# Kernel tuning notes

Hardware: AMD Instinct MI355X
Metric: run time of the kernel (lower is better)

Reference implementation:

```python
import jax, jax.numpy as jnp
import numpy as np

D_MODEL = 2048
N_HEAD = 16
N_QUERY = 2
D_HEAD = D_MODEL // (N_HEAD * N_QUERY)  # 64
KV_DIM = D_HEAD * N_HEAD                # 1024
ROPE_BASE = 10000.0


def rope(x):
    """Interleaved RoPE. theta denominator uses the RoPE module's d_model/2
    (full D_MODEL), and only the first D/2 frequencies are used for inputs of
    last dim D < D_MODEL (as in the torch code's theta[..., :d_model_2])."""
    d2_full = D_MODEL // 2
    theta = ROPE_BASE ** (-jnp.arange(d2_full, dtype=jnp.float32) / d2_full)
    S, D = x.shape[-2], x.shape[-1]
    d2 = D // 2
    ang = jnp.arange(S, dtype=jnp.float32)[:, None] * theta[:d2]  # (S, d2)
    cos, sin = jnp.cos(ang), jnp.sin(ang)
    e, o = x[..., 0::2], x[..., 1::2]
    # interleave rotated even/odd back into original layout
    return jnp.stack([e * cos - o * sin, o * cos + e * sin], axis=-1).reshape(x.shape)


def setup_inputs() -> dict:
    key = jax.random.key(0)
    ks = jax.random.split(key, 5)
    x = jax.random.normal(ks[0], (2, 2048, D_MODEL), dtype=jnp.float32)
    # weights stored as (in, out) so forward is x @ W
    Wq = jax.random.normal(ks[1], (D_MODEL, D_MODEL), dtype=jnp.float32) * 0.02
    Wk = jax.random.normal(ks[2], (D_MODEL, KV_DIM), dtype=jnp.float32) * 0.02
    Wv = jax.random.normal(ks[3], (D_MODEL, KV_DIM), dtype=jnp.float32) * 0.02
    Wo = jax.random.normal(ks[4], (D_MODEL, D_MODEL), dtype=jnp.float32) * 0.02
    return {"x": x, "Wq": Wq, "Wk": Wk, "Wv": Wv, "Wo": Wo}


def reference(x, Wq, Wk, Wv, Wo):
    b, s, _ = x.shape
    q = rope(x @ Wq)          # (b, s, D_MODEL)
    k = rope(x @ Wk)          # (b, s, KV_DIM)
    v = x @ Wv                # (b, s, KV_DIM)
    # query heads: flat head index h = g*N_QUERY + q_idx (g indexes KV head group)
    q = q.reshape(b, s, N_HEAD, N_QUERY, D_HEAD).transpose(0, 2, 3, 1, 4)  # (b,h,q,s,d)
    k = k.reshape(b, s, N_HEAD, D_HEAD)  # (b,t,h,d)
    v = v.reshape(b, s, N_HEAD, D_HEAD)
    scale = 1.0 / jnp.sqrt(jnp.asarray(D_HEAD, dtype=jnp.float32))
    scores = jnp.einsum('bhqsd,bthd->bhqst', q, k) * scale  # (b,h,q,s,t)
    probs = jax.nn.softmax(scores, axis=-1)
    out = jnp.einsum('bhqst,bthd->bhqsd', probs, v)         # (b,h,q,s,d)
    out = out.transpose(0, 3, 1, 2, 4).reshape(b, s, D_MODEL)  # (b,s,h*q*d)
    return out @ Wo
```

## Files before the change

### kernel.cpp

```cpp
#include <hip/hip_runtime.h>
#include <hip/hip_bf16.h>
#include <math.h>

#define D_MODEL 2048
#define KV_DIM  1024
#define N_HEAD  16
#define N_QUERY 2
#define D_HEAD  64
#define BATCH   2
#define SEQ     2048
#define MROWS   (BATCH * SEQ)

typedef __attribute__((ext_vector_type(8))) short short8x;
typedef __attribute__((ext_vector_type(4))) float f32x4;

__device__ __forceinline__ short f2bf_rn(float f) {
    unsigned u = __float_as_uint(f);
    unsigned r = (u + 0x7fffu + ((u >> 16) & 1u)) >> 16;
    return (short)r;
}
__device__ __forceinline__ float bf2f(short s) {
    return __uint_as_float(((unsigned)(unsigned short)s) << 16);
}

__device__ __forceinline__ void gload_lds16(const short* g, short* l) {
    __builtin_amdgcn_global_load_lds(
        (const __attribute__((address_space(1))) void*)g,
        (__attribute__((address_space(3))) void*)l,
        16, 0, 0);
}

__global__ __launch_bounds__(256)
void split_kernel(const float* __restrict__ in, short* __restrict__ h,
                  short* __restrict__ l, int n) {
    const int i = (blockIdx.x * 256 + threadIdx.x) * 4;
    if (i >= n) return;
    float4 v = *(const float4*)&in[i];
    short4 hv, lv;
    hv.x = f2bf_rn(v.x); lv.x = f2bf_rn(v.x - bf2f(hv.x));
    hv.y = f2bf_rn(v.y); lv.y = f2bf_rn(v.y - bf2f(hv.y));
    hv.z = f2bf_rn(v.z); lv.z = f2bf_rn(v.z - bf2f(hv.z));
    hv.w = f2bf_rn(v.w); lv.w = f2bf_rn(v.w - bf2f(hv.w));
    *(short4*)&h[i] = hv;
    *(short4*)&l[i] = lv;
}

__global__ __launch_bounds__(256)
void split_tr_kernel(const float* __restrict__ in, short* __restrict__ h,
                     short* __restrict__ l, int K, int N) {
    __shared__ float t[32][33];
    const int k0 = blockIdx.y * 32;
    const int n0 = blockIdx.x * 32;
    const int c  = threadIdx.x & 31;
    const int r0 = threadIdx.x >> 5;
#pragma unroll
    for (int i = 0; i < 4; ++i) {
        const int r = r0 + i * 8;
        t[r][c] = in[(size_t)(k0 + r) * N + n0 + c];
    }
    __syncthreads();
#pragma unroll
    for (int i = 0; i < 4; ++i) {
        const int r = r0 + i * 8;
        const float f = t[c][r];
        const short hb = f2bf_rn(f);
        const size_t off = (size_t)(n0 + r) * K + k0 + c;
        h[off] = hb;
        l[off] = f2bf_rn(f - bf2f(hb));
    }
}

template <int MODE>
__global__ __launch_bounds__(256)
void mgemm_bf_kernel(const short* __restrict__ Ah_g, const short* __restrict__ Al_g,
                     const short* __restrict__ Bth_g, const short* __restrict__ Btl_g,
                     float* __restrict__ C, short* __restrict__ Ch, short* __restrict__ Cl,
                     int M, int N, int K) {
    __shared__ __align__(16) short Ah[128 * 64];
    __shared__ __align__(16) short Al[128 * 64];
    __shared__ __align__(16) short Bh[128 * 64];
    __shared__ __align__(16) short Bl[128 * 64];

    const int tid  = threadIdx.x;
    const int lane = tid & 63;
    const int wid  = tid >> 6;
    const int wm   = (wid >> 1) * 64;
    const int wn   = (wid & 1) * 64;
    const int row0 = blockIdx.y * 128;
    const int col0 = blockIdx.x * 128;
    const int arow = lane & 15;
    const int kg   = lane >> 4;

    f32x4 acc[4][4];
#pragma unroll
    for (int m = 0; m < 4; ++m)
#pragma unroll
        for (int n = 0; n < 4; ++n) acc[m][n] = (f32x4)0.f;

    for (int kt = 0; kt < K; kt += 64) {
#pragma unroll
        for (int i = 0; i < 4; ++i) {
            const int c   = i * 256 + tid;
            const int r   = c >> 3;
            const int kc  = c & 7;
            const int kcs = kc ^ (r & 7);
            const int db  = (i * 256 + (tid & 192)) * 8;
            const size_t sa = (size_t)(row0 + r) * K + kt + kcs * 8;
            const size_t sb = (size_t)(col0 + r) * K + kt + kcs * 8;
            gload_lds16(&Ah_g[sa],  &Ah[db]);
            gload_lds16(&Al_g[sa],  &Al[db]);
            gload_lds16(&Bth_g[sb], &Bh[db]);
            gload_lds16(&Btl_g[sb], &Bl[db]);
        }
        __syncthreads();

#pragma unroll
        for (int kk = 0; kk < 2; ++kk) {
            const int kcb = kk * 4 + kg;
            short8x ah[4], al[4];
#pragma unroll
            for (int m = 0; m < 4; ++m) {
                const int r   = wm + m * 16 + arow;
                const int idx = r * 64 + ((kcb ^ (r & 7)) << 3);
                ah[m] = *(const short8x*)&Ah[idx];
                al[m] = *(const short8x*)&Al[idx];
            }
#pragma unroll
            for (int n = 0; n < 4; ++n) {
                const int rb   = wn + n * 16 + arow;
                const int idxb = rb * 64 + ((kcb ^ (rb & 7)) << 3);
                short8x bh = *(const short8x*)&Bh[idxb];
                short8x bl = *(const short8x*)&Bl[idxb];
#pragma unroll
                for (int m = 0; m < 4; ++m) {
                    acc[m][n] = __builtin_amdgcn_mfma_f32_16x16x32_bf16(ah[m], bl, acc[m][n], 0, 0, 0);
                    acc[m][n] = __builtin_amdgcn_mfma_f32_16x16x32_bf16(al[m], bh, acc[m][n], 0, 0, 0);
                    acc[m][n] = __builtin_amdgcn_mfma_f32_16x16x32_bf16(ah[m], bh, acc[m][n], 0, 0, 0);
                }
            }
        }
        __syncthreads();
    }

#pragma unroll
    for (int m = 0; m < 4; ++m)
#pragma unroll
        for (int n = 0; n < 4; ++n) {
            const int row = row0 + wm + m * 16 + (lane >> 4) * 4;
            const int col = col0 + wn + n * 16 + (lane & 15);
            if (MODE == 2) {
                const float v0 = acc[m][n][0], v1 = acc[m][n][1];
                const float v2 = acc[m][n][2], v3 = acc[m][n][3];
                const short h0 = f2bf_rn(v0), h1 = f2bf_rn(v1);
                const short h2 = f2bf_rn(v2), h3 = f2bf_rn(v3);
                const size_t off = (size_t)col * M + row;
                *(short4*)&Ch[off] = make_short4(h0, h1, h2, h3);
                *(short4*)&Cl[off] = make_short4(
                    f2bf_rn(v0 - bf2f(h0)), f2bf_rn(v1 - bf2f(h1)),
                    f2bf_rn(v2 - bf2f(h2)), f2bf_rn(v3 - bf2f(h3)));
            } else {
#pragma unroll
                for (int j = 0; j < 4; ++j) {
                    const size_t off = (size_t)(row + j) * N + col;
                    if (MODE == 1) {
                        const float val = acc[m][n][j];
                        const short hb = f2bf_rn(val);
                        Ch[off] = hb;
                        Cl[off] = f2bf_rn(val - bf2f(hb));
                    } else {
                        C[off] = acc[m][n][j];
                    }
                }
            }
        }
}

template <int NC, int D2>
__global__ __launch_bounds__(256)
void rope_split_kernel(short* __restrict__ h, short* __restrict__ l) {
    const int idx = blockIdx.x * 256 + threadIdx.x;
    if (idx >= MROWS * D2) return;
    const int row = idx / D2;
    const int j   = idx - row * D2;
    const int pos = row & (SEQ - 1);
    const float theta = __expf(-(float)j * (9.210340371976184f / 1024.0f));
    float s, c;
    sincosf((float)pos * theta, &s, &c);
    const size_t base = (size_t)row * NC + 2 * j;
    short2 hh = *(short2*)&h[base];
    short2 ll = *(short2*)&l[base];
    const float e = bf2f(hh.x) + bf2f(ll.x);
    const float o = bf2f(hh.y) + bf2f(ll.y);
    const float re = e * c - o * s;
    const float ro = o * c + e * s;
    const short rh0 = f2bf_rn(re), rh1 = f2bf_rn(ro);
    *(short2*)&h[base] = make_short2(rh0, rh1);
    *(short2*)&l[base] = make_short2(f2bf_rn(re - bf2f(rh0)), f2bf_rn(ro - bf2f(rh1)));
}

__global__ __launch_bounds__(256)
void attn_mfma_kernel(const short* __restrict__ qh_g, const short* __restrict__ ql_g,
                      const short* __restrict__ kh_g, const short* __restrict__ kl_g,
                      const short* __restrict__ vth_g, const short* __restrict__ vtl_g,
                      short* __restrict__ aoh, short* __restrict__ aol) {
    __shared__ __align__(16) short Qh[64 * 128], Ql[64 * 128];
    __shared__ __align__(16) short Kh[64 * 64], Kl[64 * 64];
    __shared__ __align__(16) short Vth[64 * 64], Vtl[64 * 64];
    __shared__ __align__(16) short Ph[4][16 * 64], Pl[4][16 * 64];

    const int tid  = threadIdx.x;
    const int lane = tid & 63;
    const int wid  = tid >> 6;
    const int wq   = wid * 16;
    const int arow = lane & 15;
    const int kg   = lane >> 4;

    const int y  = blockIdx.y;
    const int b  = y >> 4;
    const int h  = y & 15;
    const int qrow0 = b * SEQ + blockIdx.x * 64;
    const int hcol0 = h * (N_QUERY * D_HEAD);
    const int kvcol = h * D_HEAD;

#pragma unroll
    for (int i = 0; i < 4; ++i) {
        const int c    = i * 256 + tid;
        const int r    = c >> 4;
        const int kc2  = c & 15;
        const int kcs2 = kc2 ^ (r & 7);
        const int db   = (i * 256 + (tid & 192)) * 8;
        const size_t src = (size_t)(qrow0 + r) * D_MODEL + hcol0 + kcs2 * 8;
        gload_lds16(&qh_g[src], &Qh[db]);
        gload_lds16(&ql_g[src], &Ql[db]);
    }

    f32x4 oacc[2][4];
    float mrow[2][4], lrow[2][4];
#pragma unroll
    for (int nq = 0; nq < 2; ++nq)
#pragma unroll
        for (int t = 0; t < 4; ++t) {
            oacc[nq][t] = (f32x4)0.f;
            mrow[nq][t] = -1e30f;
            lrow[nq][t] = 0.f;
        }
    const float scale = 0.125f;
    const size_t kvrow0 = (size_t)b * SEQ;

    for (int tt = 0; tt < SEQ / 64; ++tt) {
        __syncthreads();
#pragma unroll
        for (int i = 0; i < 2; ++i) {
            const int c   = i * 256 + tid;
            const int r   = c >> 3;
            const int kc  = c & 7;
            const int kcs = kc ^ (r & 7);
            const int db  = (i * 256 + (tid & 192)) * 8;
            const size_t sk = (kvrow0 + tt * 64 + r) * KV_DIM + kvcol + kcs * 8;
            const size_t sv = (size_t)(kvcol + r) * MROWS + kvrow0 + tt * 64 + kcs * 8;
            gload_lds16(&kh_g[sk],  &Kh[db]);
            gload_lds16(&kl_g[sk],  &Kl[db]);
            gload_lds16(&vth_g[sv], &Vth[db]);
            gload_lds16(&vtl_g[sv], &Vtl[db]);
        }
        __syncthreads();

#pragma unroll
        for (int nq = 0; nq < 2; ++nq) {
            f32x4 sacc[4];
#pragma unroll
            for (int t = 0; t < 4; ++t) sacc[t] = (f32x4)0.f;
#pragma unroll
            for (int kk = 0; kk < 2; ++kk) {
                const int kcb = kk * 4 + kg;
                const int rq  = wq + arow;
                const int ia  = rq * 128 + nq * 64 + ((kcb ^ (rq & 7)) << 3);
                const short8x qh = *(const short8x*)&Qh[ia];
                const short8x ql = *(const short8x*)&Ql[ia];
#pragma unroll
                for (int t = 0; t < 4; ++t) {
                    const int rk = t * 16 + arow;
                    const int ib = rk * 64 + ((kcb ^ (rk & 7)) << 3);
                    const short8x kh = *(const short8x*)&Kh[ib];
                    const short8x kl = *(const short8x*)&Kl[ib];
                    sacc[t] = __builtin_amdgcn_mfma_f32_16x16x32_bf16(qh, kl, sacc[t], 0, 0, 0);
                    sacc[t] = __builtin_amdgcn_mfma_f32_16x16x32_bf16(ql, kh, sacc[t], 0, 0, 0);
                    sacc[t] = __builtin_amdgcn_mfma_f32_16x16x32_bf16(qh, kh, sacc[t], 0, 0, 0);
                }
            }

            float pv[4][4];
#pragma unroll
            for (int jj = 0; jj < 4; ++jj) {
                float mx = sacc[0][jj] * scale;
#pragma unroll
                for (int t = 1; t < 4; ++t) mx = fmaxf(mx, sacc[t][jj] * scale);
                mx = fmaxf(mx, __shfl_xor(mx, 1));
                mx = fmaxf(mx, __shfl_xor(mx, 2));
                mx = fmaxf(mx, __shfl_xor(mx, 4));
                mx = fmaxf(mx, __shfl_xor(mx, 8));
                const float mnew  = fmaxf(mrow[nq][jj], mx);
                const float alpha = __expf(mrow[nq][jj] - mnew);
                float ls = 0.f;
#pragma unroll
                for (int t = 0; t < 4; ++t) {
                    float p = __expf(sacc[t][jj] * scale - mnew);
                    pv[t][jj] = p;
                    ls += p;
                }
                ls += __shfl_xor(ls, 1);
                ls += __shfl_xor(ls, 2);
                ls += __shfl_xor(ls, 4);
                ls += __shfl_xor(ls, 8);
                lrow[nq][jj] = lrow[nq][jj] * alpha + ls;
                mrow[nq][jj] = mnew;
#pragma unroll
                for (int t = 0; t < 4; ++t) oacc[nq][t][jj] *= alpha;
            }

#pragma unroll
            for (int t = 0; t < 4; ++t)
#pragma unroll
                for (int jj = 0; jj < 4; ++jj) {
                    const int qq  = (lane >> 4) * 4 + jj;
                    const int kv  = t * 16 + (lane & 15);
                    const int idx = qq * 64 + (((kv >> 3) ^ (qq & 7)) << 3) + (kv & 7);
                    const short hb = f2bf_rn(pv[t][jj]);
                    Ph[wid][idx] = hb;
                    Pl[wid][idx] = f2bf_rn(pv[t][jj] - bf2f(hb));
                }
            asm volatile("s_waitcnt lgkmcnt(0)" ::: "memory");

#pragma unroll
            for (int kk = 0; kk < 2; ++kk) {
                const int kcb = kk * 4 + kg;
                const int ip  = arow * 64 + ((kcb ^ (arow & 7)) << 3);
                const short8x ph = *(const short8x*)&Ph[wid][ip];
                const short8x pl = *(const short8x*)&Pl[wid][ip];
#pragma unroll
                for (int t = 0; t < 4; ++t) {
                    const int rv = t * 16 + arow;
                    const int iv = rv * 64 + ((kcb ^ (rv & 7)) << 3);
                    const short8x vh = *(const short8x*)&Vth[iv];
                    const short8x vl = *(const short8x*)&Vtl[iv];
                    oacc[nq][t] = __builtin_amdgcn_mfma_f32_16x16x32_bf16(ph, vl, oacc[nq][t], 0, 0, 0);
                    oacc[nq][t] = __builtin_amdgcn_mfma_f32_16x16x32_bf16(pl, vh, oacc[nq][t], 0, 0, 0);
                    oacc[nq][t] = __builtin_amdgcn_mfma_f32_16x16x32_bf16(ph, vh, oacc[nq][t], 0, 0, 0);
                }
            }
        }
    }

#pragma unroll
    for (int nq = 0; nq < 2; ++nq)
#pragma unroll
        for (int jj = 0; jj < 4; ++jj) {
            const float inv = 1.f / lrow[nq][jj];
            const int row = qrow0 + wq + (lane >> 4) * 4 + jj;
#pragma unroll
            for (int t = 0; t < 4; ++t) {
                const size_t off = (size_t)row * D_MODEL + hcol0 + nq * D_HEAD
                                 + t * 16 + (lane & 15);
                const float val = oacc[nq][t][jj] * inv;
                const short hb = f2bf_rn(val);
                aoh[off] = hb;
                aol[off] = f2bf_rn(val - bf2f(hb));
            }
        }
}

extern "C" void kernel_launch(void* const* d_in, const int* in_sizes, int n_in,
                              void* d_out, int out_size, void* d_ws, size_t ws_size,
                              hipStream_t stream) {
    const float* x  = (const float*)d_in[0];
    const float* Wq = (const float*)d_in[1];
    const float* Wk = (const float*)d_in[2];
    const float* Wv = (const float*)d_in[3];
    const float* Wo = (const float*)d_in[4];
    float* out = (float*)d_out;

    const size_t MiB = (size_t)1 << 20;
    char* ws = (char*)d_ws;
    short* qh  = (short*)(ws + 0   * MiB);
    short* ql  = (short*)(ws + 16  * MiB);
    short* kh  = (short*)(ws + 32  * MiB);
    short* kl  = (short*)(ws + 40  * MiB);
    short* vth = (short*)(ws + 48  * MiB);
    short* vtl = (short*)(ws + 56  * MiB);
    short* xh  = (short*)(ws + 64  * MiB);
    short* xl  = (short*)(ws + 80  * MiB);
    short* aoh = (short*)(ws + 64  * MiB);
    short* aol = (short*)(ws + 80  * MiB);
    short* Wqh = (short*)(ws + 96  * MiB);
    short* Wql = (short*)(ws + 104 * MiB);
    short* Wkh = (short*)(ws + 112 * MiB);
    short* Wkl = (short*)(ws + 116 * MiB);
    short* Wvh = (short*)(ws + 120 * MiB);
    short* Wvl = (short*)(ws + 124 * MiB);
    short* Woh = (short*)(ws + 128 * MiB);
    short* Wol = (short*)(ws + 136 * MiB);

    split_kernel<<<(MROWS * D_MODEL) / 1024, 256, 0, stream>>>(x, xh, xl, MROWS * D_MODEL);
    split_tr_kernel<<<dim3(D_MODEL / 32, D_MODEL / 32), 256, 0, stream>>>(Wq, Wqh, Wql, D_MODEL, D_MODEL);
    split_tr_kernel<<<dim3(KV_DIM  / 32, D_MODEL / 32), 256, 0, stream>>>(Wk, Wkh, Wkl, D_MODEL, KV_DIM);
    split_tr_kernel<<<dim3(KV_DIM  / 32, D_MODEL / 32), 256, 0, stream>>>(Wv, Wvh, Wvl, D_MODEL, KV_DIM);
    split_tr_kernel<<<dim3(D_MODEL / 32, D_MODEL / 32), 256, 0, stream>>>(Wo, Woh, Wol, D_MODEL, D_MODEL);

    mgemm_bf_kernel<1><<<dim3(D_MODEL / 128, MROWS / 128), 256, 0, stream>>>(
        xh, xl, Wqh, Wql, nullptr, qh, ql, MROWS, D_MODEL, D_MODEL);
    mgemm_bf_kernel<1><<<dim3(KV_DIM / 128, MROWS / 128), 256, 0, stream>>>(
        xh, xl, Wkh, Wkl, nullptr, kh, kl, MROWS, KV_DIM, D_MODEL);
    mgemm_bf_kernel<2><<<dim3(KV_DIM / 128, MROWS / 128), 256, 0, stream>>>(
        xh, xl, Wvh, Wvl, nullptr, vth, vtl, MROWS, KV_DIM, D_MODEL);

    rope_split_kernel<D_MODEL, 1024><<<(MROWS * 1024) / 256, 256, 0, stream>>>(qh, ql);
    rope_split_kernel<KV_DIM,   512><<<(MROWS * 512)  / 256, 256, 0, stream>>>(kh, kl);

    attn_mfma_kernel<<<dim3(SEQ / 64, BATCH * N_HEAD), 256, 0, stream>>>(
        qh, ql, kh, kl, vth, vtl, aoh, aol);

    mgemm_bf_kernel<0><<<dim3(D_MODEL / 128, MROWS / 128), 256, 0, stream>>>(
        aoh, aol, Woh, Wol, out, nullptr, nullptr, MROWS, D_MODEL, D_MODEL);
}
```

Before: 826.0 us.

## Split attention query halves across eight waves and keep Q in registers

The attention kernel now launches 512 threads per block, and each wave handles one 16-row strip for one of the two query heads sharing a KV head. Previously each wave looped over both heads. Q fragments are loaded straight from global memory into registers rather than staged through LDS, which removes the Q shared buffers and the LDS reads in the inner loop. The aim is more waves in flight to hide softmax and LDS latency, with half the per-wave accumulator state so more blocks fit per CU. The cost is that each K/V tile is now shared by twice as many waves, and the wider blocks need larger P buffers.

```diff
diff --git a/kernel.cpp b/kernel.cpp
--- a/kernel.cpp
+++ b/kernel.cpp
@@ -198,20 +198,21 @@
     *(short2*)&l[base] = make_short2(f2bf_rn(re - bf2f(rh0)), f2bf_rn(ro - bf2f(rh1)));
 }
 
-__global__ __launch_bounds__(256)
+__global__ __launch_bounds__(512, 4)
 void attn_mfma_kernel(const short* __restrict__ qh_g, const short* __restrict__ ql_g,
                       const short* __restrict__ kh_g, const short* __restrict__ kl_g,
                       const short* __restrict__ vth_g, const short* __restrict__ vtl_g,
                       short* __restrict__ aoh, short* __restrict__ aol) {
-    __shared__ __align__(16) short Qh[64 * 128], Ql[64 * 128];
     __shared__ __align__(16) short Kh[64 * 64], Kl[64 * 64];
     __shared__ __align__(16) short Vth[64 * 64], Vtl[64 * 64];
-    __shared__ __align__(16) short Ph[4][16 * 64], Pl[4][16 * 64];
+    __shared__ __align__(16) short Ph[8][16 * 64], Pl[8][16 * 64];
 
     const int tid  = threadIdx.x;
     const int lane = tid & 63;
     const int wid  = tid >> 6;
-    const int wq   = wid * 16;
+    const int strip = wid >> 1;
+    const int nq    = wid & 1;
+    const int wq   = strip * 16;
     const int arow = lane & 15;
     const int kg   = lane >> 4;
 
@@ -222,40 +223,35 @@
     const int hcol0 = h * (N_QUERY * D_HEAD);
     const int kvcol = h * D_HEAD;
 
-#pragma unroll
-    for (int i = 0; i < 4; ++i) {
-        const int c    = i * 256 + tid;
-        const int r    = c >> 4;
-        const int kc2  = c & 15;
-        const int kcs2 = kc2 ^ (r & 7);
-        const int db   = (i * 256 + (tid & 192)) * 8;
-        const size_t src = (size_t)(qrow0 + r) * D_MODEL + hcol0 + kcs2 * 8;
-        gload_lds16(&qh_g[src], &Qh[db]);
-        gload_lds16(&ql_g[src], &Ql[db]);
-    }
-
-    f32x4 oacc[2][4];
-    float mrow[2][4], lrow[2][4];
-#pragma unroll
-    for (int nq = 0; nq < 2; ++nq)
-#pragma unroll
-        for (int t = 0; t < 4; ++t) {
-            oacc[nq][t] = (f32x4)0.f;
-            mrow[nq][t] = -1e30f;
-            lrow[nq][t] = 0.f;
-        }
+    short8x qhr[2], qlr[2];
+    {
+        const size_t qbase = (size_t)(qrow0 + wq + arow) * D_MODEL + hcol0 + nq * D_HEAD;
+#pragma unroll
+        for (int kk = 0; kk < 2; ++kk) {
+            const int kcb = kk * 4 + kg;
+            qhr[kk] = *(const short8x*)&qh_g[qbase + kcb * 8];
+            qlr[kk] = *(const short8x*)&ql_g[qbase + kcb * 8];
+        }
+    }
+
+    f32x4 oacc[4];
+    float mrow[4], lrow[4];
+#pragma unroll
+    for (int t = 0; t < 4; ++t) {
+        oacc[t] = (f32x4)0.f;
+        mrow[t] = -1e30f;
+        lrow[t] = 0.f;
+    }
     const float scale = 0.125f;
     const size_t kvrow0 = (size_t)b * SEQ;
 
     for (int tt = 0; tt < SEQ / 64; ++tt) {
         __syncthreads();
-#pragma unroll
-        for (int i = 0; i < 2; ++i) {
-            const int c   = i * 256 + tid;
-            const int r   = c >> 3;
-            const int kc  = c & 7;
+        {
+            const int r   = tid >> 3;
+            const int kc  = tid & 7;
             const int kcs = kc ^ (r & 7);
-            const int db  = (i * 256 + (tid & 192)) * 8;
+            const int db  = (tid & 448) * 8;
             const size_t sk = (kvrow0 + tt * 64 + r) * KV_DIM + kvcol + kcs * 8;
             const size_t sv = (size_t)(kvcol + r) * MROWS + kvrow0 + tt * 64 + kcs * 8;
             gload_lds16(&kh_g[sk],  &Kh[db]);
@@ -265,108 +261,101 @@
         }
         __syncthreads();
 
-#pragma unroll
-        for (int nq = 0; nq < 2; ++nq) {
-            f32x4 sacc[4];
-#pragma unroll
-            for (int t = 0; t < 4; ++t) sacc[t] = (f32x4)0.f;
-#pragma unroll
-            for (int kk = 0; kk < 2; ++kk) {
-                const int kcb = kk * 4 + kg;
-                const int rq  = wq + arow;
-                const int ia  = rq * 128 + nq * 64 + ((kcb ^ (rq & 7)) << 3);
-                const short8x qh = *(const short8x*)&Qh[ia];
-                const short8x ql = *(const short8x*)&Ql[ia];
-#pragma unroll
-                for (int t = 0; t < 4; ++t) {
-                    const int rk = t * 16 + arow;
-                    const int ib = rk * 64 + ((kcb ^ (rk & 7)) << 3);
-                    const short8x kh = *(const short8x*)&Kh[ib];
-                    const short8x kl = *(const short8x*)&Kl[ib];
-                    sacc[t] = __builtin_amdgcn_mfma_f32_16x16x32_bf16(qh, kl, sacc[t], 0, 0, 0);
-                    sacc[t] = __builtin_amdgcn_mfma_f32_16x16x32_bf16(ql, kh, sacc[t], 0, 0, 0);
-                    sacc[t] = __builtin_amdgcn_mfma_f32_16x16x32_bf16(qh, kh, sacc[t], 0, 0, 0);
-                }
-            }
-
-            float pv[4][4];
+        f32x4 sacc[4];
+#pragma unroll
+        for (int t = 0; t < 4; ++t) sacc[t] = (f32x4)0.f;
+#pragma unroll
+        for (int kk = 0; kk < 2; ++kk) {
+            const int kcb = kk * 4 + kg;
+            const short8x qh = qhr[kk];
+            const short8x ql = qlr[kk];
+#pragma unroll
+            for (int t = 0; t < 4; ++t) {
+                const int rk = t * 16 + arow;
+                const int ib = rk * 64 + ((kcb ^ (rk & 7)) << 3);
+                const short8x kh = *(const short8x*)&Kh[ib];
+                const short8x kl = *(const short8x*)&Kl[ib];
+                sacc[t] = __builtin_amdgcn_mfma_f32_16x16x32_bf16(qh, kl, sacc[t], 0, 0, 0);
+                sacc[t] = __builtin_amdgcn_mfma_f32_16x16x32_bf16(ql, kh, sacc[t], 0, 0, 0);
+                sacc[t] = __builtin_amdgcn_mfma_f32_16x16x32_bf16(qh, kh, sacc[t], 0, 0, 0);
+            }
+        }
+
+        float pv[4][4];
+#pragma unroll
+        for (int jj = 0; jj < 4; ++jj) {
+            float mx = sacc[0][jj] * scale;
+#pragma unroll
+            for (int t = 1; t < 4; ++t) mx = fmaxf(mx, sacc[t][jj] * scale);
+            mx = fmaxf(mx, __shfl_xor(mx, 1));
+            mx = fmaxf(mx, __shfl_xor(mx, 2));
+            mx = fmaxf(mx, __shfl_xor(mx, 4));
+            mx = fmaxf(mx, __shfl_xor(mx, 8));
+            const float mnew  = fmaxf(mrow[jj], mx);
+            const float alpha = __expf(mrow[jj] - mnew);
+            float ls = 0.f;
+#pragma unroll
+            for (int t = 0; t < 4; ++t) {
+                float p = __expf(sacc[t][jj] * scale - mnew);
+                pv[t][jj] = p;
+                ls += p;
+            }
+            ls += __shfl_xor(ls, 1);
+            ls += __shfl_xor(ls, 2);
+            ls += __shfl_xor(ls, 4);
+            ls += __shfl_xor(ls, 8);
+            lrow[jj] = lrow[jj] * alpha + ls;
+            mrow[jj] = mnew;
+#pragma unroll
+            for (int t = 0; t < 4; ++t) oacc[t][jj] *= alpha;
+        }
+
+#pragma unroll
+        for (int t = 0; t < 4; ++t)
 #pragma unroll
             for (int jj = 0; jj < 4; ++jj) {
-                float mx = sacc[0][jj] * scale;
-#pragma unroll
-                for (int t = 1; t < 4; ++t) mx = fmaxf(mx, sacc[t][jj] * scale);
-                mx = fmaxf(mx, __shfl_xor(mx, 1));
-                mx = fmaxf(mx, __shfl_xor(mx, 2));
-                mx = fmaxf(mx, __shfl_xor(mx, 4));
-                mx = fmaxf(mx, __shfl_xor(mx, 8));
-                const float mnew  = fmaxf(mrow[nq][jj], mx);
-                const float alpha = __expf(mrow[nq][jj] - mnew);
-                float ls = 0.f;
-#pragma unroll
-                for (int t = 0; t < 4; ++t) {
-                    float p = __expf(sacc[t][jj] * scale - mnew);
-                    pv[t][jj] = p;
-                    ls += p;
-                }
-                ls += __shfl_xor(ls, 1);
-                ls += __shfl_xor(ls, 2);
-                ls += __shfl_xor(ls, 4);
-                ls += __shfl_xor(ls, 8);
-                lrow[nq][jj] = lrow[nq][jj] * alpha + ls;
-                mrow[nq][jj] = mnew;
-#pragma unroll
-                for (int t = 0; t < 4; ++t) oacc[nq][t][jj] *= alpha;
-            }
-
-#pragma unroll
-            for (int t = 0; t < 4; ++t)
-#pragma unroll
-                for (int jj = 0; jj < 4; ++jj) {
-                    const int qq  = (lane >> 4) * 4 + jj;
-                    const int kv  = t * 16 + (lane & 15);
-                    const int idx = qq * 64 + (((kv >> 3) ^ (qq & 7)) << 3) + (kv & 7);
-                    const short hb = f2bf_rn(pv[t][jj]);
-                    Ph[wid][idx] = hb;
-                    Pl[wid][idx] = f2bf_rn(pv[t][jj] - bf2f(hb));
-                }
-            asm volatile("s_waitcnt lgkmcnt(0)" ::: "memory");
-
-#pragma unroll
-            for (int kk = 0; kk < 2; ++kk) {
-                const int kcb = kk * 4 + kg;
-                const int ip  = arow * 64 + ((kcb ^ (arow & 7)) << 3);
-                const short8x ph = *(const short8x*)&Ph[wid][ip];
-                const short8x pl = *(const short8x*)&Pl[wid][ip];
-#pragma unroll
-                for (int t = 0; t < 4; ++t) {
-                    const int rv = t * 16 + arow;
-                    const int iv = rv * 64 + ((kcb ^ (rv & 7)) << 3);
-                    const short8x vh = *(const short8x*)&Vth[iv];
-                    const short8x vl = *(const short8x*)&Vtl[iv];
-                    oacc[nq][t] = __builtin_amdgcn_mfma_f32_16x16x32_bf16(ph, vl, oacc[nq][t], 0, 0, 0);
-                    oacc[nq][t] = __builtin_amdgcn_mfma_f32_16x16x32_bf16(pl, vh, oacc[nq][t], 0, 0, 0);
-                    oacc[nq][t] = __builtin_amdgcn_mfma_f32_16x16x32_bf16(ph, vh, oacc[nq][t], 0, 0, 0);
-                }
-            }
-        }
-    }
-
-#pragma unroll
-    for (int nq = 0; nq < 2; ++nq)
-#pragma unroll
-        for (int jj = 0; jj < 4; ++jj) {
-            const float inv = 1.f / lrow[nq][jj];
-            const int row = qrow0 + wq + (lane >> 4) * 4 + jj;
+                const int qq  = (lane >> 4) * 4 + jj;
+                const int kv  = t * 16 + (lane & 15);
+                const int idx = qq * 64 + (((kv >> 3) ^ (qq & 7)) << 3) + (kv & 7);
+                const short hb = f2bf_rn(pv[t][jj]);
+                Ph[wid][idx] = hb;
+                Pl[wid][idx] = f2bf_rn(pv[t][jj] - bf2f(hb));
+            }
+        asm volatile("s_waitcnt lgkmcnt(0)" ::: "memory");
+
+#pragma unroll
+        for (int kk = 0; kk < 2; ++kk) {
+            const int kcb = kk * 4 + kg;
+            const int ip  = arow * 64 + ((kcb ^ (arow & 7)) << 3);
+            const short8x ph = *(const short8x*)&Ph[wid][ip];
+            const short8x pl = *(const short8x*)&Pl[wid][ip];
 #pragma unroll
             for (int t = 0; t < 4; ++t) {
-                const size_t off = (size_t)row * D_MODEL + hcol0 + nq * D_HEAD
-                                 + t * 16 + (lane & 15);
-                const float val = oacc[nq][t][jj] * inv;
-                const short hb = f2bf_rn(val);
-                aoh[off] = hb;
-                aol[off] = f2bf_rn(val - bf2f(hb));
-            }
-        }
+                const int rv = t * 16 + arow;
+                const int iv = rv * 64 + ((kcb ^ (rv & 7)) << 3);
+                const short8x vh = *(const short8x*)&Vth[iv];
+                const short8x vl = *(const short8x*)&Vtl[iv];
+                oacc[t] = __builtin_amdgcn_mfma_f32_16x16x32_bf16(ph, vl, oacc[t], 0, 0, 0);
+                oacc[t] = __builtin_amdgcn_mfma_f32_16x16x32_bf16(pl, vh, oacc[t], 0, 0, 0);
+                oacc[t] = __builtin_amdgcn_mfma_f32_16x16x32_bf16(ph, vh, oacc[t], 0, 0, 0);
+            }
+        }
+    }
+
+#pragma unroll
+    for (int jj = 0; jj < 4; ++jj) {
+        const float inv = 1.f / lrow[jj];
+        const int row = qrow0 + wq + (lane >> 4) * 4 + jj;
+#pragma unroll
+        for (int t = 0; t < 4; ++t) {
+            const size_t off = (size_t)row * D_MODEL + hcol0 + nq * D_HEAD
+                             + t * 16 + (lane & 15);
+            const float val = oacc[t][jj] * inv;
+            const short hb = f2bf_rn(val);
+            aoh[off] = hb;
+            aol[off] = f2bf_rn(val - bf2f(hb));
+        }
+    }
 }
 
 extern "C" void kernel_launch(void* const* d_in, const int* in_sizes, int n_in,
@@ -416,7 +405,7 @@
     rope_split_kernel<D_MODEL, 1024><<<(MROWS * 1024) / 256, 256, 0, stream>>>(qh, ql);
     rope_split_kernel<KV_DIM,   512><<<(MROWS * 512)  / 256, 256, 0, stream>>>(kh, kl);
 
-    attn_mfma_kernel<<<dim3(SEQ / 64, BATCH * N_HEAD), 256, 0, stream>>>(
+    attn_mfma_kernel<<<dim3(SEQ / 64, BATCH * N_HEAD), 512, 0, stream>>>(
         qh, ql, kh, kl, vth, vtl, aoh, aol);
 
     mgemm_bf_kernel<0><<<dim3(D_MODEL / 128, MROWS / 128), 256, 0, stream>>>(
```

After: 793.7 us. 3.9% less time.
